# Optimization experiments

Hardware: AMD Instinct MI355X
Metric: run time of the kernel (lower is better)

Reference implementation:

```python
import jax, jax.numpy as jnp
import numpy as np

N, E, IN, H, B, OUT = 50000, 800000, 256, 64, 4096, 2
EPS, NEG = 0.3, 0.3  # eps residual coeff, LeakyReLU negative slope


def _xav(key, shape, gain=1.414):
    std = gain * np.sqrt(2.0 / (shape[0] + shape[1]))
    return jax.random.normal(key, shape, jnp.float32) * np.float32(std)


def setup_inputs():
    key = jax.random.key(0)
    ks = jax.random.split(key, 32)
    inp = {}
    inp["h"] = jax.random.normal(ks[0], (N, IN), jnp.float32)
    for i, name in enumerate(["src1", "dst1", "src2", "dst2", "src3", "dst3"]):
        inp[name] = jax.random.randint(ks[1 + i], (E,), 0, N, jnp.int32)
    inp["nodes"] = jax.random.randint(ks[7], (B,), 0, N, jnp.int32)
    inp["t1_w"] = _xav(ks[8], (H, IN))
    inp["t1_b"] = jnp.zeros((H,), jnp.float32)
    for i in range(3):
        inp[f"gw1_{i+1}"] = _xav(ks[9 + i], (1, 2 * H))
        inp[f"gb1_{i+1}"] = jnp.zeros((1,), jnp.float32)
        inp[f"hw1_{i+1}"] = _xav(ks[12 + i], (H, H))
        inp[f"gw2_{i+1}"] = _xav(ks[15 + i], (1, 6 * H))
        inp[f"gb2_{i+1}"] = jnp.zeros((1,), jnp.float32)
        inp[f"hw2_{i+1}"] = _xav(ks[18 + i], (3 * H, H))
    inp["t2_w"] = _xav(ks[21], (64, 7 * H + IN))
    inp["t2_b"] = jnp.zeros((64,), jnp.float32)
    inp["t3_w"] = _xav(ks[22], (OUT, 64))
    inp["t3_b"] = jnp.zeros((OUT,), jnp.float32)
    return inp


def _leaky(x):
    return jnp.where(x >= 0, x, NEG * x)


def _deg_norm(dst):
    # symmetric degree normalization d_i = 1/sqrt(deg_i) (FAGCN-style ndata['d'])
    deg = jax.ops.segment_sum(jnp.ones(dst.shape, jnp.float32), dst, num_segments=N)
    return jnp.where(deg > 0, jax.lax.rsqrt(jnp.maximum(deg, 1.0)), 0.0)


def _layer(h, src, dst, gw, gb, d):
    # a = tanh(gate(cat[h_dst, h_src])): split gate weight to avoid [E,2D] concat
    D = h.shape[1]
    a = jnp.tanh(h[dst] @ gw[0, :D] + h[src] @ gw[0, D:] + gb[0])  # [E]
    e = a * d[dst] * d[src]                                        # [E]
    # z_i = sum_{(src->i)} h_src * e  (DGL u_mul_e + sum)
    return jax.ops.segment_sum(h[src] * e[:, None], dst, num_segments=N)


def reference(h, t1_w, t1_b,
              gw1_1, gb1_1, hw1_1, gw1_2, gb1_2, hw1_2, gw1_3, gb1_3, hw1_3,
              gw2_1, gb2_1, hw2_1, gw2_2, gb2_2, hw2_2, gw2_3, gb2_3, hw2_3,
              t2_w, t2_b, t3_w, t3_b,
              src1, dst1, src2, dst2, src3, dst3, nodes):
    d1, d2, d3 = _deg_norm(dst1), _deg_norm(dst2), _deg_norm(dst3)
    raw0 = h
    x = _leaky(h @ t1_w.T + t1_b)                   # [N, H]
    raw1 = x
    h1_1 = _leaky((EPS * raw1 + _layer(x, src1, dst1, gw1_1, gb1_1, d1)) @ hw1_1)
    h1_2 = _leaky((EPS * raw1 + _layer(x, src2, dst2, gw1_2, gb1_2, d2)) @ hw1_2)
    h1_3 = _leaky((EPS * raw1 + _layer(x, src3, dst3, gw1_3, gb1_3, d3)) @ hw1_3)
    raw2 = jnp.concatenate([h1_1, h1_2, h1_3], axis=1)  # [N, 3H]
    h2_1 = _leaky((EPS * raw2 + _layer(raw2, src1, dst1, gw2_1, gb2_1, d1)) @ hw2_1)
    h2_2 = _leaky((EPS * raw2 + _layer(raw2, src2, dst2, gw2_2, gb2_2, d2)) @ hw2_2)
    h2_3 = _leaky((EPS * raw2 + _layer(raw2, src3, dst3, gw2_3, gb2_3, d3)) @ hw2_3)
    final = jnp.concatenate([h2_1, h2_2, h2_3, raw0, raw1, raw2], axis=1)  # [N, 7H+IN]
    nf = final[nodes]                                # [B, 7H+IN]
    s64 = _leaky(nf @ t2_w.T + t2_b)                 # [B, 64]
    scores = s64 @ t3_w.T + t3_b                     # [B, OUT]
    return scores, s64
```

## Files before the change

kernel.cpp:

```cpp
#include <hip/hip_runtime.h>

#define NN 50000
#define EE 800000
#define BB 4096
#define NB 512
#define BW 98
#define CAP 2176
#define CH 128

#define OFF_T1W 0
#define OFF_T1B 16384
#define OFF_GW1 16448
#define OFF_GB1 16832
#define OFF_HW1 16848
#define OFF_GW2 29136
#define OFF_GB2 30288
#define OFF_HW2 30304
#define OFF_T2W 67168
#define OFF_T2B 112224
#define OFF_T3W 112288
#define OFF_T3B 112416
#define WTOT    112418

#define WB_T1W  0
#define WB_HW1T 16384
#define WB_HW2T 28672
#define WB_T2W  65536
#define WB_TOT  110592

typedef __attribute__((ext_vector_type(8))) short bf16x8;
typedef __attribute__((ext_vector_type(4))) float f32x4;

__device__ __forceinline__ float bf2f(unsigned short u) {
    return __uint_as_float(((unsigned int)u) << 16);
}
__device__ __forceinline__ unsigned short f2bf(float f) {
    unsigned int u = __float_as_uint(f);
    u = (u + 0x7fffu + ((u >> 16) & 1u)) >> 16;
    return (unsigned short)u;
}
__device__ __forceinline__ float leakyf(float v) { return v >= 0.f ? v : 0.3f * v; }
__device__ __forceinline__ float tanh_fast(float v) {
    float e = __expf(2.f * v);
    return 1.f - 2.f / (e + 1.f);
}
__device__ __forceinline__ int rfl(int v) { return __builtin_amdgcn_readfirstlane(v); }

__global__ void k_sniff(const unsigned short* __restrict__ hs, int* __restrict__ flag) {
    int lane = threadIdx.x;
    unsigned short s = hs[2 * lane];
    int ef = (s >> 7) & 0xFF;
    unsigned long long m = __ballot(ef >= 100 && ef <= 132);
    if (lane == 0) flag[0] = (__popcll(m) >= 40) ? 0 : 1;
}

__global__ __launch_bounds__(1024) void k_convert(
    const int* __restrict__ fl,
    const void* t1w, const void* t1b,
    const void* gw1a, const void* gw1b, const void* gw1c,
    const void* gb1a, const void* gb1b, const void* gb1c,
    const void* hw1a, const void* hw1b, const void* hw1c,
    const void* gw2a, const void* gw2b, const void* gw2c,
    const void* gb2a, const void* gb2b, const void* gb2c,
    const void* hw2a, const void* hw2b, const void* hw2c,
    const void* t2w, const void* t2b, const void* t3w, const void* t3b,
    float* __restrict__ fw) {
    const int starts[24] = {0, 16384, 16448, 16576, 16704, 16832, 16833, 16834,
                            16848, 20944, 25040, 29136, 29520, 29904, 30288, 30289, 30290,
                            30304, 42592, 54880, 67168, 112224, 112288, 112416};
    const int cnts[24] = {16384, 64, 128, 128, 128, 1, 1, 1, 4096, 4096, 4096,
                          384, 384, 384, 1, 1, 1, 12288, 12288, 12288, 45056, 64, 128, 2};
    const void* sp[24] = {t1w, t1b, gw1a, gw1b, gw1c, gb1a, gb1b, gb1c, hw1a, hw1b, hw1c,
                          gw2a, gw2b, gw2c, gb2a, gb2b, gb2c, hw2a, hw2b, hw2c, t2w, t2b, t3w, t3b};
    int isf32 = fl[0];
    int idx = blockIdx.x * 1024 + threadIdx.x;
    if (idx >= WTOT) return;
    float v = 0.f;
#pragma unroll
    for (int k = 0; k < 24; ++k) {
        int lo = idx - starts[k];
        if (lo >= 0 && lo < cnts[k])
            v = isf32 ? ((const float*)sp[k])[lo] : bf2f(((const unsigned short*)sp[k])[lo]);
    }
    fw[idx] = v;
}

__global__ __launch_bounds__(256) void k_convert16(const int* __restrict__ fl, const void* t1w,
                                                   const void* hw1a, const void* hw1b, const void* hw1c,
                                                   const void* hw2a, const void* hw2b, const void* hw2c,
                                                   const void* t2w, unsigned short* __restrict__ wb) {
    int idx = blockIdx.x * 256 + threadIdx.x;
    if (idx >= WB_TOT) return;
    int isf32 = fl[0];
    const void* p;
    int srci;
    if (idx < WB_HW1T) {
        p = t1w; srci = idx;
    } else if (idx < WB_HW2T) {
        int rel = idx - WB_HW1T;
        int set = rel >> 12, r2 = rel & 4095;
        int jj = r2 >> 6, kk = r2 & 63;
        p = set == 0 ? hw1a : (set == 1 ? hw1b : hw1c);
        srci = kk * 64 + jj;
    } else if (idx < WB_T2W) {
        int rel = idx - WB_HW2T;
        int set = rel / 12288, r2 = rel % 12288;
        int n = r2 / 192, k = r2 % 192;
        p = set == 0 ? hw2a : (set == 1 ? hw2b : hw2c);
        srci = k * 64 + n;
    } else {
        p = t2w; srci = idx - WB_T2W;
    }
    wb[idx] = isf32 ? f2bf(((const float*)p)[srci]) : ((const unsigned short*)p)[srci];
}

__global__ __launch_bounds__(256) void k_bucketA(const int* __restrict__ s0, const int* __restrict__ s1,
                                                 const int* __restrict__ s2, const int* __restrict__ d0,
                                                 const int* __restrict__ d1, const int* __restrict__ d2,
                                                 int* __restrict__ gcur, unsigned int* __restrict__ tmp) {
    int set = blockIdx.y;
    const int* ss = set == 0 ? s0 : (set == 1 ? s1 : s2);
    const int* dd = set == 0 ? d0 : (set == 1 ? d1 : d2);
    __shared__ int hist[NB];
    __shared__ int lcur[NB];
    int tid = threadIdx.x;
    for (int i = tid; i < NB; i += 256) { hist[i] = 0; lcur[i] = 0; }
    __syncthreads();
    int e0 = blockIdx.x * (EE / CH);
    int e1 = e0 + (EE / CH);
    for (int t = e0 + tid; t < e1; t += 256)
        atomicAdd(&hist[dd[t] / BW], 1);
    __syncthreads();
    for (int b = tid; b < NB; b += 256) {
        int hh = hist[b];
        if (hh > 0) hist[b] = atomicAdd(&gcur[set * NB + b], hh);
    }
    __syncthreads();
    unsigned int* tp = tmp + (size_t)set * NB * CAP;
    for (int t = e0 + tid; t < e1; t += 256) {
        int d = dd[t], s = ss[t];
        int b = d / BW;
        int r = atomicAdd(&lcur[b], 1);
        int pos = hist[b] + r;
        if (pos < CAP) tp[(size_t)b * CAP + pos] = (unsigned)s | ((unsigned)(d - b * BW) << 16);
    }
}

__global__ __launch_bounds__(256) void k_rowptr(const int* __restrict__ gcur,
                                                const unsigned int* __restrict__ tmp,
                                                int* __restrict__ deg, int* __restrict__ rowptr,
                                                float* __restrict__ g1, float* __restrict__ g2) {
    int b = blockIdx.x, set = blockIdx.y;
    int nb = b * BW;
    if (nb >= NN) return;
    __shared__ int hist[BW];
    __shared__ int rp[BW];
    int tid = threadIdx.x;
    int nv = NN - nb < BW ? NN - nb : BW;
    if (tid < BW) hist[tid] = 0;
    __syncthreads();
    int cnt = gcur[set * NB + b];
    if (cnt > CAP) cnt = CAP;
    const unsigned int* tp = tmp + (size_t)set * NB * CAP + (size_t)b * CAP;
    for (int j = tid; j < cnt; j += 256) atomicAdd(&hist[tp[j] >> 16], 1);
    __syncthreads();
    if (tid == 0) {
        int run = 0;
        for (int i = 0; i < nv; ++i) { rp[i] = run; run += hist[i]; }
    }
    __syncthreads();
    if (tid < nv) {
        int dg = hist[tid];
        size_t n = (size_t)set * NN + nb + tid;
        deg[n] = dg;
        rowptr[n] = b * CAP + rp[tid];
        float v = dg > 0 ? rsqrtf((float)dg) : 0.f;
        g1[n * 4 + 2] = v;
        g2[n * 4 + 2] = v;
    }
}

__global__ __launch_bounds__(256) void k_input(const int* __restrict__ fl,
                                               const void* __restrict__ hB,
                                               const unsigned short* __restrict__ wb,
                                               const float* __restrict__ fw,
                                               unsigned short* __restrict__ x16,
                                               float4* __restrict__ g1v4) {
    __shared__ float xt[16][65];
    int tid = threadIdx.x, lane = tid & 63, wid = tid >> 6;
    int m = lane & 15, q = lane >> 4;
    int node0 = blockIdx.x * 16;
    int isf32 = fl[0];
    f32x4 acc = {0.f, 0.f, 0.f, 0.f};
    const unsigned short* bsrc = wb + WB_T1W + ((size_t)(wid * 16 + m)) * 256 + q * 8;
    if (isf32) {
        const float* ap = (const float*)hB + (size_t)(node0 + m) * 256 + q * 8;
        for (int k0 = 0; k0 < 256; k0 += 32) {
            float4 f0 = *(const float4*)(ap + k0);
            float4 f1 = *(const float4*)(ap + k0 + 4);
            bf16x8 a;
            a[0] = (short)f2bf(f0.x); a[1] = (short)f2bf(f0.y);
            a[2] = (short)f2bf(f0.z); a[3] = (short)f2bf(f0.w);
            a[4] = (short)f2bf(f1.x); a[5] = (short)f2bf(f1.y);
            a[6] = (short)f2bf(f1.z); a[7] = (short)f2bf(f1.w);
            bf16x8 b = *(const bf16x8*)(bsrc + k0);
            acc = __builtin_amdgcn_mfma_f32_16x16x32_bf16(a, b, acc, 0, 0, 0);
        }
    } else {
        const unsigned short* ap = (const unsigned short*)hB + (size_t)(node0 + m) * 256 + q * 8;
        for (int k0 = 0; k0 < 256; k0 += 32) {
            bf16x8 a = *(const bf16x8*)(ap + k0);
            bf16x8 b = *(const bf16x8*)(bsrc + k0);
            acc = __builtin_amdgcn_mfma_f32_16x16x32_bf16(a, b, acc, 0, 0, 0);
        }
    }
    int gcol = wid * 16 + m;
    float bias = fw[OFF_T1B + gcol];
#pragma unroll
    for (int r = 0; r < 4; ++r) {
        int row = q * 4 + r;
        float v = leakyf(acc[r] + bias);
        x16[(size_t)(node0 + row) * 64 + gcol] = f2bf(v);
        xt[row][gcol] = v;
    }
    __syncthreads();
    int nl = wid * 4 + q;
    int node = node0 + nl;
    float xv[4];
#pragma unroll
    for (int r = 0; r < 4; ++r) xv[r] = xt[nl][m + 16 * r];
#pragma unroll
    for (int set = 0; set < 3; ++set) {
        const float* gw = fw + OFF_GW1 + set * 128;
        float pd = 0.f, ps = 0.f;
#pragma unroll
        for (int r = 0; r < 4; ++r) {
            int c = m + 16 * r;
            pd = fmaf(xv[r], gw[c], pd);
            ps = fmaf(xv[r], gw[64 + c], ps);
        }
        pd += __shfl_xor(pd, 1); ps += __shfl_xor(ps, 1);
        pd += __shfl_xor(pd, 2); ps += __shfl_xor(ps, 2);
        pd += __shfl_xor(pd, 4); ps += __shfl_xor(ps, 4);
        pd += __shfl_xor(pd, 8); ps += __shfl_xor(ps, 8);
        if (m == 0) {
            float2* p = (float2*)&g1v4[(size_t)set * NN + node];
            *p = make_float2(ps, pd);
        }
    }
}

__global__ __launch_bounds__(256) void k_bucketB(const int* __restrict__ gcur,
                                                 const unsigned int* __restrict__ tmp,
                                                 const int* __restrict__ rowptr,
                                                 const float4* __restrict__ g1v4,
                                                 const float* __restrict__ fw,
                                                 unsigned int* __restrict__ csr) {
    int b = blockIdx.x, set = blockIdx.y;
    int nb = b * BW;
    if (nb >= NN) return;
    __shared__ float4 gdw[BW];
    __shared__ int cur[BW];
    __shared__ int rpl[BW];
    int tid = threadIdx.x;
    int nv = NN - nb < BW ? NN - nb : BW;
    if (tid < nv) {
        gdw[tid] = g1v4[(size_t)set * NN + nb + tid];
        rpl[tid] = rowptr[(size_t)set * NN + nb + tid];
        cur[tid] = 0;
    }
    __syncthreads();
    int cnt = gcur[set * NB + b];
    if (cnt > CAP) cnt = CAP;
    float gbv = fw[OFF_GB1 + set];
    const float4* gv = g1v4 + (size_t)set * NN;
    const unsigned int* tp = tmp + (size_t)set * NB * CAP + (size_t)b * CAP;
    unsigned int* cp = csr + (size_t)set * NB * CAP;
    for (int j = tid; j < cnt; j += 256) {
        unsigned rec = tp[j];
        int s = rec & 0xFFFF;
        int dl = rec >> 16;
        float4 gs = gv[s];
        float4 gd = gdw[dl];
        float a = tanh_fast(gd.y + gs.x + gbv);
        float e = a * gd.z * gs.z;
        int rank = atomicAdd(&cur[dl], 1);
        cp[rpl[dl] + rank] = (unsigned)s | ((unsigned)f2bf(e) << 16);
    }
}

__global__ __launch_bounds__(1024) void k_layer1(const unsigned short* __restrict__ x16,
                                                 const unsigned int* __restrict__ csr,
                                                 const int* __restrict__ rowptr,
                                                 const int* __restrict__ deg,
                                                 const float* __restrict__ fw,
                                                 const unsigned short* __restrict__ wb,
                                                 unsigned short* __restrict__ raw2_16,
                                                 float4* __restrict__ g2v4) {
    __shared__ unsigned short tb[3][16][72];
    __shared__ unsigned short r2l[16][200];
    int tid = threadIdx.x, lane = tid & 63, wid = tid >> 6;
    int half = lane >> 5, c = lane & 31;
    int node = blockIdx.x * 16 + wid;
    unsigned xres = *(const unsigned*)(x16 + (size_t)node * 64 + 2 * c);
    float xr0 = bf2f((unsigned short)(xres & 0xFFFF));
    float xr1 = bf2f((unsigned short)(xres >> 16));
#pragma unroll
    for (int set = 0; set < 3; ++set) {
        int start = rfl(rowptr[(size_t)set * NN + node]);
        int cnt = rfl(deg[(size_t)set * NN + node]);
        const unsigned int* cs = csr + (size_t)set * NB * CAP + start;
        float a0 = 0.f, a1 = 0.f;
        int j = 0;
        for (; j + 8 <= cnt; j += 8) {
#pragma unroll
            for (int k = 0; k < 4; ++k) {
                unsigned rec = cs[j + 2 * k + half];
                float e = bf2f((unsigned short)(rec >> 16));
                unsigned u = *(const unsigned*)(x16 + (size_t)(rec & 0xFFFF) * 64 + 2 * c);
                a0 = fmaf(bf2f((unsigned short)(u & 0xFFFF)), e, a0);
                a1 = fmaf(bf2f((unsigned short)(u >> 16)), e, a1);
            }
        }
        for (; j + 2 <= cnt; j += 2) {
            unsigned rec = cs[j + half];
            float e = bf2f((unsigned short)(rec >> 16));
            unsigned u = *(const unsigned*)(x16 + (size_t)(rec & 0xFFFF) * 64 + 2 * c);
            a0 = fmaf(bf2f((unsigned short)(u & 0xFFFF)), e, a0);
            a1 = fmaf(bf2f((unsigned short)(u >> 16)), e, a1);
        }
        if (j < cnt && half == 0) {
            unsigned rec = cs[j];
            float e = bf2f((unsigned short)(rec >> 16));
            unsigned u = *(const unsigned*)(x16 + (size_t)(rec & 0xFFFF) * 64 + 2 * c);
            a0 = fmaf(bf2f((unsigned short)(u & 0xFFFF)), e, a0);
            a1 = fmaf(bf2f((unsigned short)(u >> 16)), e, a1);
        }
        a0 += __shfl_xor(a0, 32);
        a1 += __shfl_xor(a1, 32);
        if (half == 0) {
            unsigned p = ((unsigned)f2bf(fmaf(0.3f, xr1, a1)) << 16) |
                         (unsigned)f2bf(fmaf(0.3f, xr0, a0));
            *(unsigned*)&tb[set][wid][2 * c] = p;
        }
    }
    __syncthreads();
    int m = lane & 15, q = lane >> 4;
    if (wid < 12) {
        int set = wid >> 2, sw = wid & 3;
        f32x4 c4 = {0.f, 0.f, 0.f, 0.f};
        const unsigned short* bp = wb + WB_HW1T + set * 4096 + (sw * 16 + m) * 64 + q * 8;
#pragma unroll
        for (int k0 = 0; k0 < 64; k0 += 32) {
            bf16x8 a = *(const bf16x8*)&tb[set][m][k0 + q * 8];
            bf16x8 b = *(const bf16x8*)(bp + k0);
            c4 = __builtin_amdgcn_mfma_f32_16x16x32_bf16(a, b, c4, 0, 0, 0);
        }
        int gcol = sw * 16 + m;
#pragma unroll
        for (int r = 0; r < 4; ++r) {
            int row = q * 4 + r;
            unsigned short v = f2bf(leakyf(c4[r]));
            raw2_16[(size_t)(blockIdx.x * 16 + row) * 192 + set * 64 + gcol] = v;
            r2l[row][set * 64 + gcol] = v;
        }
    }
    __syncthreads();
    float pd[3] = {0.f, 0.f, 0.f}, ps[3] = {0.f, 0.f, 0.f};
    float rv[3];
#pragma unroll
    for (int t = 0; t < 3; ++t) rv[t] = bf2f(r2l[wid][lane * 3 + t]);
#pragma unroll
    for (int set = 0; set < 3; ++set) {
        const float* g = fw + OFF_GW2 + set * 384;
#pragma unroll
        for (int t = 0; t < 3; ++t) {
            int cc = lane * 3 + t;
            pd[set] = fmaf(rv[t], g[cc], pd[set]);
            ps[set] = fmaf(rv[t], g[192 + cc], ps[set]);
        }
    }
#pragma unroll
    for (int mm = 32; mm >= 1; mm >>= 1) {
#pragma unroll
        for (int set = 0; set < 3; ++set) {
            pd[set] += __shfl_xor(pd[set], mm);
            ps[set] += __shfl_xor(ps[set], mm);
        }
    }
    if (lane == 0) {
#pragma unroll
        for (int set = 0; set < 3; ++set) {
            float2* p = (float2*)&g2v4[(size_t)set * NN + node];
            *p = make_float2(ps[set], pd[set]);
        }
    }
}

__global__ __launch_bounds__(256) void k_mark(const int* __restrict__ nodes, int* __restrict__ mark,
                                              int* __restrict__ slotof, int* __restrict__ slotnode,
                                              int* __restrict__ cnt) {
    int b = blockIdx.x * 256 + threadIdx.x;
    if (b < BB) {
        int n = nodes[b];
        if (atomicCAS(&mark[n], 0, 1) == 0) {
            int s = atomicAdd(cnt, 1);
            slotof[n] = s;
            slotnode[s] = n;
        }
    }
}

__global__ __launch_bounds__(1024) void k_layer2(const unsigned short* __restrict__ raw2_16,
                                                 const unsigned int* __restrict__ csr,
                                                 const int* __restrict__ rowptr,
                                                 const int* __restrict__ deg,
                                                 const float4* __restrict__ g2v4,
                                                 const float* __restrict__ fw,
                                                 const int* __restrict__ slotnode,
                                                 const int* __restrict__ cntp,
                                                 float* __restrict__ z2) {
    int set = blockIdx.y;
    int tid = threadIdx.x, lane = tid & 63, wid = tid >> 6;
    int half = lane >> 5, c = lane & 31;
    int slot = blockIdx.x * 16 + wid;
    if (slot >= cntp[0]) return;
    int node = rfl(slotnode[slot]);
    int start = rfl(rowptr[(size_t)set * NN + node]);
    int cnt = rfl(deg[(size_t)set * NN + node]);
    float4 gn = g2v4[(size_t)set * NN + node];
    float pdv = gn.y, dnd = gn.z;
    float gbv = fw[OFF_GB2 + set];
    const unsigned int* cs = csr + (size_t)set * NB * CAP + start;
    const float4* gv = g2v4 + (size_t)set * NN;
    float a[6] = {0.f, 0.f, 0.f, 0.f, 0.f, 0.f};
    int j = 0;
    for (; j + 2 <= cnt; j += 2) {
        unsigned rec = cs[j + half];
        int s = rec & 0xFFFF;
        float4 g = gv[s];
        float e = tanh_fast(pdv + g.x + gbv) * dnd * g.z;
        const unsigned short* r = raw2_16 + (size_t)s * 192;
#pragma unroll
        for (int blk = 0; blk < 3; ++blk) {
            unsigned u = *(const unsigned*)(r + blk * 64 + 2 * c);
            a[2 * blk] = fmaf(bf2f((unsigned short)(u & 0xFFFF)), e, a[2 * blk]);
            a[2 * blk + 1] = fmaf(bf2f((unsigned short)(u >> 16)), e, a[2 * blk + 1]);
        }
    }
    if (j < cnt && half == 0) {
        unsigned rec = cs[j];
        int s = rec & 0xFFFF;
        float4 g = gv[s];
        float e = tanh_fast(pdv + g.x + gbv) * dnd * g.z;
        const unsigned short* r = raw2_16 + (size_t)s * 192;
#pragma unroll
        for (int blk = 0; blk < 3; ++blk) {
            unsigned u = *(const unsigned*)(r + blk * 64 + 2 * c);
            a[2 * blk] = fmaf(bf2f((unsigned short)(u & 0xFFFF)), e, a[2 * blk]);
            a[2 * blk + 1] = fmaf(bf2f((unsigned short)(u >> 16)), e, a[2 * blk + 1]);
        }
    }
#pragma unroll
    for (int i = 0; i < 6; ++i) a[i] += __shfl_xor(a[i], 32);
    if (half == 0) {
        float* z = z2 + (size_t)slot * 576 + (size_t)set * 192;
#pragma unroll
        for (int blk = 0; blk < 3; ++blk) {
            z[blk * 64 + 2 * c] = a[2 * blk];
            z[blk * 64 + 2 * c + 1] = a[2 * blk + 1];
        }
    }
}

__global__ __launch_bounds__(256) void k_final(const int* __restrict__ fl,
                                               const int* __restrict__ nodes,
                                               const int* __restrict__ slotof,
                                               const float* __restrict__ z2,
                                               const unsigned short* __restrict__ raw2_16,
                                               const unsigned short* __restrict__ x16,
                                               const void* __restrict__ hB,
                                               const float* __restrict__ fw,
                                               const unsigned short* __restrict__ wb,
                                               void* __restrict__ outv) {
    __shared__ unsigned short nfb[16][712];
    __shared__ unsigned short tbb[16][200];
    __shared__ float sarr[16][64];
    __shared__ int nd[16], sl[16];
    int tid = threadIdx.x, lane = tid & 63, wid = tid >> 6;
    int m = lane & 15, q = lane >> 4;
    int b0 = blockIdx.x * 16;
    int isf32 = fl[0];
    if (tid < 16) {
        int n = nodes[b0 + tid];
        nd[tid] = n;
        sl[tid] = slotof[n];
    }
    __syncthreads();
    for (int idx = tid; idx < 16 * 256; idx += 256) {
        int row = idx >> 8, c = idx & 255;
        size_t hi = (size_t)nd[row] * 256 + c;
        nfb[row][192 + c] = isf32 ? f2bf(((const float*)hB)[hi]) : ((const unsigned short*)hB)[hi];
    }
    for (int idx = tid; idx < 16 * 64; idx += 256) {
        int row = idx >> 6, c = idx & 63;
        nfb[row][448 + c] = x16[(size_t)nd[row] * 64 + c];
    }
    for (int idx = tid; idx < 16 * 192; idx += 256) {
        int row = idx / 192, c = idx % 192;
        nfb[row][512 + c] = raw2_16[(size_t)nd[row] * 192 + c];
    }
    for (int set = 0; set < 3; ++set) {
        __syncthreads();
        for (int idx = tid; idx < 16 * 192; idx += 256) {
            int row = idx / 192, c = idx % 192;
            float r2 = bf2f(nfb[row][512 + c]);
            tbb[row][c] = f2bf(fmaf(0.3f, r2, z2[(size_t)sl[row] * 576 + set * 192 + c]));
        }
        __syncthreads();
        f32x4 c4 = {0.f, 0.f, 0.f, 0.f};
        const unsigned short* bp = wb + WB_HW2T + set * 12288 + (wid * 16 + m) * 192 + q * 8;
#pragma unroll
        for (int k0 = 0; k0 < 192; k0 += 32) {
            bf16x8 a = *(const bf16x8*)&tbb[m][k0 + q * 8];
            bf16x8 bf = *(const bf16x8*)(bp + k0);
            c4 = __builtin_amdgcn_mfma_f32_16x16x32_bf16(a, bf, c4, 0, 0, 0);
        }
        int col = wid * 16 + m;
#pragma unroll
        for (int r = 0; r < 4; ++r)
            nfb[q * 4 + r][set * 64 + col] = f2bf(leakyf(c4[r]));
    }
    __syncthreads();
    f32x4 c4 = {0.f, 0.f, 0.f, 0.f};
    const unsigned short* bp = wb + WB_T2W + (wid * 16 + m) * 704 + q * 8;
#pragma unroll
    for (int k0 = 0; k0 < 704; k0 += 32) {
        bf16x8 a = *(const bf16x8*)&nfb[m][k0 + q * 8];
        bf16x8 bf = *(const bf16x8*)(bp + k0);
        c4 = __builtin_amdgcn_mfma_f32_16x16x32_bf16(a, bf, c4, 0, 0, 0);
    }
    int col = wid * 16 + m;
    float bias = fw[OFF_T2B + col];
#pragma unroll
    for (int r = 0; r < 4; ++r) {
        int row = q * 4 + r;
        float sv = leakyf(c4[r] + bias);
        sarr[row][col] = sv;
        size_t oi = 8192 + (size_t)(b0 + row) * 64 + col;
        if (isf32) ((float*)outv)[oi] = sv;
        else ((unsigned short*)outv)[oi] = f2bf(sv);
    }
    __syncthreads();
    if (tid < 32) {
        int row = tid >> 1, oc = tid & 1;
        float acc2 = fw[OFF_T3B + oc];
        const float* tw = fw + OFF_T3W + oc * 64;
#pragma unroll 8
        for (int c = 0; c < 64; ++c) acc2 = fmaf(sarr[row][c], tw[c], acc2);
        size_t oi = (size_t)(b0 + row) * 2 + oc;
        if (isf32) ((float*)outv)[oi] = acc2;
        else ((unsigned short*)outv)[oi] = f2bf(acc2);
    }
}

extern "C" void kernel_launch(void* const* d_in, const int* in_sizes, int n_in,
                              void* d_out, int out_size, void* d_ws, size_t ws_size,
                              hipStream_t stream) {
    const void* h = d_in[0];
    const int* src1 = (const int*)d_in[1];
    const int* dst1 = (const int*)d_in[2];
    const int* src2 = (const int*)d_in[3];
    const int* dst2 = (const int*)d_in[4];
    const int* src3 = (const int*)d_in[5];
    const int* dst3 = (const int*)d_in[6];
    const int* nodes = (const int*)d_in[7];

    char* w = (char*)d_ws;
    size_t off = 0;
    auto carve = [&](size_t bytes) -> void* {
        void* p = w + off;
        off += (bytes + 255) & ~(size_t)255;
        return p;
    };
    int* flag = (int*)carve(256);
    int* gcur = (int*)carve((size_t)3 * NB * 4);
    int* mark = (int*)carve((size_t)NN * 4);
    int* cntp = (int*)carve(256);
    int* deg = (int*)carve((size_t)3 * NN * 4);
    int* rowptr = (int*)carve((size_t)3 * NN * 4);
    float4* g1v4 = (float4*)carve((size_t)3 * NN * 16);
    float4* g2v4 = (float4*)carve((size_t)3 * NN * 16);
    unsigned int* tmp = (unsigned int*)carve((size_t)3 * NB * CAP * 4);
    unsigned int* csr = (unsigned int*)carve((size_t)3 * NB * CAP * 4);
    float* fw = (float*)carve((size_t)WTOT * 4);
    unsigned short* wb = (unsigned short*)carve((size_t)WB_TOT * 2);
    unsigned short* x16 = (unsigned short*)carve((size_t)NN * 64 * 2);
    unsigned short* raw2_16 = (unsigned short*)carve((size_t)NN * 192 * 2);
    int* slotof = (int*)carve((size_t)NN * 4);
    int* slotnode = (int*)carve((size_t)BB * 4);
    float* z2 = (float*)carve((size_t)BB * 576 * 4);

    size_t zbytes = (size_t)((char*)cntp - (char*)gcur) + 256;
    hipMemsetAsync(gcur, 0, zbytes, stream);

    k_sniff<<<1, 64, 0, stream>>>((const unsigned short*)h, flag);
    k_convert<<<(WTOT + 1023) / 1024, 1024, 0, stream>>>(
        flag, d_in[8], d_in[9],
        d_in[10], d_in[16], d_in[22],
        d_in[11], d_in[17], d_in[23],
        d_in[12], d_in[18], d_in[24],
        d_in[13], d_in[19], d_in[25],
        d_in[14], d_in[20], d_in[26],
        d_in[15], d_in[21], d_in[27],
        d_in[28], d_in[29], d_in[30], d_in[31], fw);
    k_convert16<<<(WB_TOT + 255) / 256, 256, 0, stream>>>(flag, d_in[8],
                                                          d_in[12], d_in[18], d_in[24],
                                                          d_in[15], d_in[21], d_in[27],
                                                          d_in[28], wb);

    dim3 gch(CH, 3);
    k_bucketA<<<gch, 256, 0, stream>>>(src1, src2, src3, dst1, dst2, dst3, gcur, tmp);
    dim3 gb(NB, 3);
    k_rowptr<<<gb, 256, 0, stream>>>(gcur, tmp, deg, rowptr, (float*)g1v4, (float*)g2v4);

    k_input<<<3125, 256, 0, stream>>>(flag, h, wb, fw, x16, g1v4);
    k_bucketB<<<gb, 256, 0, stream>>>(gcur, tmp, rowptr, g1v4, fw, csr);
    k_mark<<<(BB + 255) / 256, 256, 0, stream>>>(nodes, mark, slotof, slotnode, cntp);

    k_layer1<<<3125, 1024, 0, stream>>>(x16, csr, rowptr, deg, fw, wb, raw2_16, g2v4);
    dim3 gl2(BB / 16, 3);
    k_layer2<<<gl2, 1024, 0, stream>>>(raw2_16, csr, rowptr, deg, g2v4, fw, slotnode, cntp, z2);
    k_final<<<BB / 16, 256, 0, stream>>>(flag, nodes, slotof, z2, raw2_16, x16, h, fw, wb, d_out);
}
```

Before: 413.6 us.

## Fuse layer-2 aggregation into final kernel, merge convert kernels, inline dtype sniff

Folds the dtype sniff into each kernel that needs it, merges the two weight-conversion kernels into one launch, and drops the dedup/mark pass. Layer-2 aggregation now runs directly inside the final kernel per batch node, with no z2 round-trip. Layer-1 aggregation is regathered with 8-byte loads and 4 edges per wave step. This cuts launches, the memset and z2 traffic, at the cost of recomputing aggregation for duplicate batch nodes and running fewer blocks in the final kernel.

```diff
diff --git a/kernel.cpp b/kernel.cpp
--- a/kernel.cpp
+++ b/kernel.cpp
@@ -21,6 +21,7 @@
 #define OFF_T3W 112288
 #define OFF_T3B 112416
 #define WTOT    112418
+#define WPAD    112640
 
 #define WB_T1W  0
 #define WB_HW1T 16384
@@ -46,16 +47,16 @@
 }
 __device__ __forceinline__ int rfl(int v) { return __builtin_amdgcn_readfirstlane(v); }
 
-__global__ void k_sniff(const unsigned short* __restrict__ hs, int* __restrict__ flag) {
-    int lane = threadIdx.x;
+__device__ __forceinline__ int sniff_wave(const unsigned short* hs) {
+    int lane = threadIdx.x & 63;
     unsigned short s = hs[2 * lane];
     int ef = (s >> 7) & 0xFF;
     unsigned long long m = __ballot(ef >= 100 && ef <= 132);
-    if (lane == 0) flag[0] = (__popcll(m) >= 40) ? 0 : 1;
-}
-
-__global__ __launch_bounds__(1024) void k_convert(
-    const int* __restrict__ fl,
+    return (__popcll(m) >= 40) ? 0 : 1;
+}
+
+__global__ __launch_bounds__(256) void k_convert(
+    const unsigned short* __restrict__ hs,
     const void* t1w, const void* t1b,
     const void* gw1a, const void* gw1b, const void* gw1c,
     const void* gb1a, const void* gb1b, const void* gb1c,
@@ -64,7 +65,7 @@
     const void* gb2a, const void* gb2b, const void* gb2c,
     const void* hw2a, const void* hw2b, const void* hw2c,
     const void* t2w, const void* t2b, const void* t3w, const void* t3b,
-    float* __restrict__ fw) {
+    float* __restrict__ fw, unsigned short* __restrict__ wb) {
     const int starts[24] = {0, 16384, 16448, 16576, 16704, 16832, 16833, 16834,
                             16848, 20944, 25040, 29136, 29520, 29904, 30288, 30289, 30290,
                             30304, 42592, 54880, 67168, 112224, 112288, 112416};
@@ -72,46 +73,40 @@
                           384, 384, 384, 1, 1, 1, 12288, 12288, 12288, 45056, 64, 128, 2};
     const void* sp[24] = {t1w, t1b, gw1a, gw1b, gw1c, gb1a, gb1b, gb1c, hw1a, hw1b, hw1c,
                           gw2a, gw2b, gw2c, gb2a, gb2b, gb2c, hw2a, hw2b, hw2c, t2w, t2b, t3w, t3b};
-    int isf32 = fl[0];
-    int idx = blockIdx.x * 1024 + threadIdx.x;
-    if (idx >= WTOT) return;
-    float v = 0.f;
-#pragma unroll
-    for (int k = 0; k < 24; ++k) {
-        int lo = idx - starts[k];
-        if (lo >= 0 && lo < cnts[k])
-            v = isf32 ? ((const float*)sp[k])[lo] : bf2f(((const unsigned short*)sp[k])[lo]);
-    }
-    fw[idx] = v;
-}
-
-__global__ __launch_bounds__(256) void k_convert16(const int* __restrict__ fl, const void* t1w,
-                                                   const void* hw1a, const void* hw1b, const void* hw1c,
-                                                   const void* hw2a, const void* hw2b, const void* hw2c,
-                                                   const void* t2w, unsigned short* __restrict__ wb) {
+    int isf32 = sniff_wave(hs);
     int idx = blockIdx.x * 256 + threadIdx.x;
-    if (idx >= WB_TOT) return;
-    int isf32 = fl[0];
-    const void* p;
-    int srci;
-    if (idx < WB_HW1T) {
-        p = t1w; srci = idx;
-    } else if (idx < WB_HW2T) {
-        int rel = idx - WB_HW1T;
-        int set = rel >> 12, r2 = rel & 4095;
-        int jj = r2 >> 6, kk = r2 & 63;
-        p = set == 0 ? hw1a : (set == 1 ? hw1b : hw1c);
-        srci = kk * 64 + jj;
-    } else if (idx < WB_T2W) {
-        int rel = idx - WB_HW2T;
-        int set = rel / 12288, r2 = rel % 12288;
-        int n = r2 / 192, k = r2 % 192;
-        p = set == 0 ? hw2a : (set == 1 ? hw2b : hw2c);
-        srci = k * 64 + n;
-    } else {
-        p = t2w; srci = idx - WB_T2W;
-    }
-    wb[idx] = isf32 ? f2bf(((const float*)p)[srci]) : ((const unsigned short*)p)[srci];
+    if (idx < WTOT) {
+        float v = 0.f;
+#pragma unroll
+        for (int k = 0; k < 24; ++k) {
+            int lo = idx - starts[k];
+            if (lo >= 0 && lo < cnts[k])
+                v = isf32 ? ((const float*)sp[k])[lo] : bf2f(((const unsigned short*)sp[k])[lo]);
+        }
+        fw[idx] = v;
+    } else if (idx >= WPAD && idx < WPAD + WB_TOT) {
+        int i2 = idx - WPAD;
+        const void* p;
+        int srci;
+        if (i2 < WB_HW1T) {
+            p = t1w; srci = i2;
+        } else if (i2 < WB_HW2T) {
+            int rel = i2 - WB_HW1T;
+            int set = rel >> 12, r2 = rel & 4095;
+            int jj = r2 >> 6, kk = r2 & 63;
+            p = set == 0 ? hw1a : (set == 1 ? hw1b : hw1c);
+            srci = kk * 64 + jj;
+        } else if (i2 < WB_T2W) {
+            int rel = i2 - WB_HW2T;
+            int set = rel / 12288, r2 = rel % 12288;
+            int n = r2 / 192, k = r2 % 192;
+            p = set == 0 ? hw2a : (set == 1 ? hw2b : hw2c);
+            srci = k * 64 + n;
+        } else {
+            p = t2w; srci = i2 - WB_T2W;
+        }
+        wb[i2] = isf32 ? f2bf(((const float*)p)[srci]) : ((const unsigned short*)p)[srci];
+    }
 }
 
 __global__ __launch_bounds__(256) void k_bucketA(const int* __restrict__ s0, const int* __restrict__ s1,
@@ -180,8 +175,7 @@
     }
 }
 
-__global__ __launch_bounds__(256) void k_input(const int* __restrict__ fl,
-                                               const void* __restrict__ hB,
+__global__ __launch_bounds__(256) void k_input(const void* __restrict__ hB,
                                                const unsigned short* __restrict__ wb,
                                                const float* __restrict__ fw,
                                                unsigned short* __restrict__ x16,
@@ -190,7 +184,7 @@
     int tid = threadIdx.x, lane = tid & 63, wid = tid >> 6;
     int m = lane & 15, q = lane >> 4;
     int node0 = blockIdx.x * 16;
-    int isf32 = fl[0];
+    int isf32 = sniff_wave((const unsigned short*)hB);
     f32x4 acc = {0.f, 0.f, 0.f, 0.f};
     const unsigned short* bsrc = wb + WB_T1W + ((size_t)(wid * 16 + m)) * 256 + q * 8;
     if (isf32) {
@@ -300,48 +294,54 @@
     __shared__ unsigned short tb[3][16][72];
     __shared__ unsigned short r2l[16][200];
     int tid = threadIdx.x, lane = tid & 63, wid = tid >> 6;
-    int half = lane >> 5, c = lane & 31;
+    int g = lane >> 4, f = lane & 15;
     int node = blockIdx.x * 16 + wid;
-    unsigned xres = *(const unsigned*)(x16 + (size_t)node * 64 + 2 * c);
-    float xr0 = bf2f((unsigned short)(xres & 0xFFFF));
-    float xr1 = bf2f((unsigned short)(xres >> 16));
 #pragma unroll
     for (int set = 0; set < 3; ++set) {
         int start = rfl(rowptr[(size_t)set * NN + node]);
         int cnt = rfl(deg[(size_t)set * NN + node]);
         const unsigned int* cs = csr + (size_t)set * NB * CAP + start;
-        float a0 = 0.f, a1 = 0.f;
+        float a0 = 0.f, a1 = 0.f, a2 = 0.f, a3 = 0.f;
         int j = 0;
         for (; j + 8 <= cnt; j += 8) {
 #pragma unroll
-            for (int k = 0; k < 4; ++k) {
-                unsigned rec = cs[j + 2 * k + half];
+            for (int k2 = 0; k2 < 2; ++k2) {
+                unsigned rec = cs[j + 4 * k2 + g];
                 float e = bf2f((unsigned short)(rec >> 16));
-                unsigned u = *(const unsigned*)(x16 + (size_t)(rec & 0xFFFF) * 64 + 2 * c);
-                a0 = fmaf(bf2f((unsigned short)(u & 0xFFFF)), e, a0);
-                a1 = fmaf(bf2f((unsigned short)(u >> 16)), e, a1);
+                uint2 u = *(const uint2*)(x16 + (size_t)(rec & 0xFFFF) * 64 + 4 * f);
+                a0 = fmaf(bf2f((unsigned short)(u.x & 0xFFFF)), e, a0);
+                a1 = fmaf(bf2f((unsigned short)(u.x >> 16)), e, a1);
+                a2 = fmaf(bf2f((unsigned short)(u.y & 0xFFFF)), e, a2);
+                a3 = fmaf(bf2f((unsigned short)(u.y >> 16)), e, a3);
             }
         }
-        for (; j + 2 <= cnt; j += 2) {
-            unsigned rec = cs[j + half];
-            float e = bf2f((unsigned short)(rec >> 16));
-            unsigned u = *(const unsigned*)(x16 + (size_t)(rec & 0xFFFF) * 64 + 2 * c);
-            a0 = fmaf(bf2f((unsigned short)(u & 0xFFFF)), e, a0);
-            a1 = fmaf(bf2f((unsigned short)(u >> 16)), e, a1);
-        }
-        if (j < cnt && half == 0) {
-            unsigned rec = cs[j];
-            float e = bf2f((unsigned short)(rec >> 16));
-            unsigned u = *(const unsigned*)(x16 + (size_t)(rec & 0xFFFF) * 64 + 2 * c);
-            a0 = fmaf(bf2f((unsigned short)(u & 0xFFFF)), e, a0);
-            a1 = fmaf(bf2f((unsigned short)(u >> 16)), e, a1);
-        }
-        a0 += __shfl_xor(a0, 32);
-        a1 += __shfl_xor(a1, 32);
-        if (half == 0) {
-            unsigned p = ((unsigned)f2bf(fmaf(0.3f, xr1, a1)) << 16) |
-                         (unsigned)f2bf(fmaf(0.3f, xr0, a0));
-            *(unsigned*)&tb[set][wid][2 * c] = p;
+#pragma unroll
+        for (int t = 0; t < 2; ++t) {
+            int idx = j + 4 * t + g;
+            if (idx < cnt) {
+                unsigned rec = cs[idx];
+                float e = bf2f((unsigned short)(rec >> 16));
+                uint2 u = *(const uint2*)(x16 + (size_t)(rec & 0xFFFF) * 64 + 4 * f);
+                a0 = fmaf(bf2f((unsigned short)(u.x & 0xFFFF)), e, a0);
+                a1 = fmaf(bf2f((unsigned short)(u.x >> 16)), e, a1);
+                a2 = fmaf(bf2f((unsigned short)(u.y & 0xFFFF)), e, a2);
+                a3 = fmaf(bf2f((unsigned short)(u.y >> 16)), e, a3);
+            }
+        }
+        a0 += __shfl_xor(a0, 16); a0 += __shfl_xor(a0, 32);
+        a1 += __shfl_xor(a1, 16); a1 += __shfl_xor(a1, 32);
+        a2 += __shfl_xor(a2, 16); a2 += __shfl_xor(a2, 32);
+        a3 += __shfl_xor(a3, 16); a3 += __shfl_xor(a3, 32);
+        if (g == 0) {
+            uint2 ur = *(const uint2*)(x16 + (size_t)node * 64 + 4 * f);
+            float t0 = fmaf(0.3f, bf2f((unsigned short)(ur.x & 0xFFFF)), a0);
+            float t1 = fmaf(0.3f, bf2f((unsigned short)(ur.x >> 16)), a1);
+            float t2 = fmaf(0.3f, bf2f((unsigned short)(ur.y & 0xFFFF)), a2);
+            float t3 = fmaf(0.3f, bf2f((unsigned short)(ur.y >> 16)), a3);
+            uint2 pk;
+            pk.x = (unsigned)f2bf(t0) | ((unsigned)f2bf(t1) << 16);
+            pk.y = (unsigned)f2bf(t2) | ((unsigned)f2bf(t3) << 16);
+            *(uint2*)&tb[set][wid][4 * f] = pk;
         }
     }
     __syncthreads();
@@ -372,12 +372,12 @@
     for (int t = 0; t < 3; ++t) rv[t] = bf2f(r2l[wid][lane * 3 + t]);
 #pragma unroll
     for (int set = 0; set < 3; ++set) {
-        const float* g = fw + OFF_GW2 + set * 384;
+        const float* gg = fw + OFF_GW2 + set * 384;
 #pragma unroll
         for (int t = 0; t < 3; ++t) {
             int cc = lane * 3 + t;
-            pd[set] = fmaf(rv[t], g[cc], pd[set]);
-            ps[set] = fmaf(rv[t], g[192 + cc], ps[set]);
+            pd[set] = fmaf(rv[t], gg[cc], pd[set]);
+            ps[set] = fmaf(rv[t], gg[192 + cc], ps[set]);
         }
     }
 #pragma unroll
@@ -397,159 +397,132 @@
     }
 }
 
-__global__ __launch_bounds__(256) void k_mark(const int* __restrict__ nodes, int* __restrict__ mark,
-                                              int* __restrict__ slotof, int* __restrict__ slotnode,
-                                              int* __restrict__ cnt) {
-    int b = blockIdx.x * 256 + threadIdx.x;
-    if (b < BB) {
-        int n = nodes[b];
-        if (atomicCAS(&mark[n], 0, 1) == 0) {
-            int s = atomicAdd(cnt, 1);
-            slotof[n] = s;
-            slotnode[s] = n;
-        }
-    }
-}
-
-__global__ __launch_bounds__(1024) void k_layer2(const unsigned short* __restrict__ raw2_16,
-                                                 const unsigned int* __restrict__ csr,
-                                                 const int* __restrict__ rowptr,
-                                                 const int* __restrict__ deg,
-                                                 const float4* __restrict__ g2v4,
-                                                 const float* __restrict__ fw,
-                                                 const int* __restrict__ slotnode,
-                                                 const int* __restrict__ cntp,
-                                                 float* __restrict__ z2) {
-    int set = blockIdx.y;
+__global__ __launch_bounds__(1024) void k_final(const int* __restrict__ nodes,
+                                                const unsigned short* __restrict__ raw2_16,
+                                                const unsigned short* __restrict__ x16,
+                                                const void* __restrict__ hB,
+                                                const unsigned int* __restrict__ csr,
+                                                const int* __restrict__ rowptr,
+                                                const int* __restrict__ deg,
+                                                const float4* __restrict__ g2v4,
+                                                const float* __restrict__ fw,
+                                                const unsigned short* __restrict__ wb,
+                                                void* __restrict__ outv) {
+    __shared__ unsigned short nfb[16][712];
+    __shared__ unsigned short tbb3[16][584];
+    __shared__ float sarr[16][64];
+    __shared__ int nd[16];
     int tid = threadIdx.x, lane = tid & 63, wid = tid >> 6;
-    int half = lane >> 5, c = lane & 31;
-    int slot = blockIdx.x * 16 + wid;
-    if (slot >= cntp[0]) return;
-    int node = rfl(slotnode[slot]);
-    int start = rfl(rowptr[(size_t)set * NN + node]);
-    int cnt = rfl(deg[(size_t)set * NN + node]);
-    float4 gn = g2v4[(size_t)set * NN + node];
-    float pdv = gn.y, dnd = gn.z;
-    float gbv = fw[OFF_GB2 + set];
-    const unsigned int* cs = csr + (size_t)set * NB * CAP + start;
-    const float4* gv = g2v4 + (size_t)set * NN;
-    float a[6] = {0.f, 0.f, 0.f, 0.f, 0.f, 0.f};
-    int j = 0;
-    for (; j + 2 <= cnt; j += 2) {
-        unsigned rec = cs[j + half];
-        int s = rec & 0xFFFF;
-        float4 g = gv[s];
-        float e = tanh_fast(pdv + g.x + gbv) * dnd * g.z;
-        const unsigned short* r = raw2_16 + (size_t)s * 192;
-#pragma unroll
-        for (int blk = 0; blk < 3; ++blk) {
-            unsigned u = *(const unsigned*)(r + blk * 64 + 2 * c);
-            a[2 * blk] = fmaf(bf2f((unsigned short)(u & 0xFFFF)), e, a[2 * blk]);
-            a[2 * blk + 1] = fmaf(bf2f((unsigned short)(u >> 16)), e, a[2 * blk + 1]);
-        }
-    }
-    if (j < cnt && half == 0) {
-        unsigned rec = cs[j];
-        int s = rec & 0xFFFF;
-        float4 g = gv[s];
-        float e = tanh_fast(pdv + g.x + gbv) * dnd * g.z;
-        const unsigned short* r = raw2_16 + (size_t)s * 192;
-#pragma unroll
-        for (int blk = 0; blk < 3; ++blk) {
-            unsigned u = *(const unsigned*)(r + blk * 64 + 2 * c);
-            a[2 * blk] = fmaf(bf2f((unsigned short)(u & 0xFFFF)), e, a[2 * blk]);
-            a[2 * blk + 1] = fmaf(bf2f((unsigned short)(u >> 16)), e, a[2 * blk + 1]);
-        }
-    }
-#pragma unroll
-    for (int i = 0; i < 6; ++i) a[i] += __shfl_xor(a[i], 32);
-    if (half == 0) {
-        float* z = z2 + (size_t)slot * 576 + (size_t)set * 192;
-#pragma unroll
-        for (int blk = 0; blk < 3; ++blk) {
-            z[blk * 64 + 2 * c] = a[2 * blk];
-            z[blk * 64 + 2 * c + 1] = a[2 * blk + 1];
-        }
-    }
-}
-
-__global__ __launch_bounds__(256) void k_final(const int* __restrict__ fl,
-                                               const int* __restrict__ nodes,
-                                               const int* __restrict__ slotof,
-                                               const float* __restrict__ z2,
-                                               const unsigned short* __restrict__ raw2_16,
-                                               const unsigned short* __restrict__ x16,
-                                               const void* __restrict__ hB,
-                                               const float* __restrict__ fw,
-                                               const unsigned short* __restrict__ wb,
-                                               void* __restrict__ outv) {
-    __shared__ unsigned short nfb[16][712];
-    __shared__ unsigned short tbb[16][200];
-    __shared__ float sarr[16][64];
-    __shared__ int nd[16], sl[16];
-    int tid = threadIdx.x, lane = tid & 63, wid = tid >> 6;
-    int m = lane & 15, q = lane >> 4;
     int b0 = blockIdx.x * 16;
-    int isf32 = fl[0];
-    if (tid < 16) {
-        int n = nodes[b0 + tid];
-        nd[tid] = n;
-        sl[tid] = slotof[n];
-    }
-    __syncthreads();
-    for (int idx = tid; idx < 16 * 256; idx += 256) {
+    int isf32 = sniff_wave((const unsigned short*)hB);
+    if (tid < 16) nd[tid] = nodes[b0 + tid];
+    __syncthreads();
+    for (int idx = tid; idx < 16 * 256; idx += 1024) {
         int row = idx >> 8, c = idx & 255;
         size_t hi = (size_t)nd[row] * 256 + c;
         nfb[row][192 + c] = isf32 ? f2bf(((const float*)hB)[hi]) : ((const unsigned short*)hB)[hi];
     }
-    for (int idx = tid; idx < 16 * 64; idx += 256) {
+    for (int idx = tid; idx < 16 * 64; idx += 1024) {
         int row = idx >> 6, c = idx & 63;
         nfb[row][448 + c] = x16[(size_t)nd[row] * 64 + c];
     }
-    for (int idx = tid; idx < 16 * 192; idx += 256) {
+    for (int idx = tid; idx < 16 * 192; idx += 1024) {
         int row = idx / 192, c = idx % 192;
         nfb[row][512 + c] = raw2_16[(size_t)nd[row] * 192 + c];
     }
-    for (int set = 0; set < 3; ++set) {
-        __syncthreads();
-        for (int idx = tid; idx < 16 * 192; idx += 256) {
-            int row = idx / 192, c = idx % 192;
-            float r2 = bf2f(nfb[row][512 + c]);
-            tbb[row][c] = f2bf(fmaf(0.3f, r2, z2[(size_t)sl[row] * 576 + set * 192 + c]));
-        }
-        __syncthreads();
+    __syncthreads();
+    {
+        int node = rfl(nd[wid]);
+        int half = lane >> 5, c = lane & 31;
+#pragma unroll
+        for (int set = 0; set < 3; ++set) {
+            int start = rfl(rowptr[(size_t)set * NN + node]);
+            int cnt = rfl(deg[(size_t)set * NN + node]);
+            float4 gn = g2v4[(size_t)set * NN + node];
+            float pdv = gn.y, dnd = gn.z;
+            float gbv = fw[OFF_GB2 + set];
+            const unsigned int* cs = csr + (size_t)set * NB * CAP + start;
+            const float4* gv = g2v4 + (size_t)set * NN;
+            float a[6] = {0.f, 0.f, 0.f, 0.f, 0.f, 0.f};
+            int j = 0;
+            for (; j + 2 <= cnt; j += 2) {
+                unsigned rec = cs[j + half];
+                int s = rec & 0xFFFF;
+                float4 gg = gv[s];
+                float e = tanh_fast(pdv + gg.x + gbv) * dnd * gg.z;
+                const unsigned short* r = raw2_16 + (size_t)s * 192;
+#pragma unroll
+                for (int blk = 0; blk < 3; ++blk) {
+                    unsigned u = *(const unsigned*)(r + blk * 64 + 2 * c);
+                    a[2 * blk] = fmaf(bf2f((unsigned short)(u & 0xFFFF)), e, a[2 * blk]);
+                    a[2 * blk + 1] = fmaf(bf2f((unsigned short)(u >> 16)), e, a[2 * blk + 1]);
+                }
+            }
+            if (j < cnt && half == 0) {
+                unsigned rec = cs[j];
+                int s = rec & 0xFFFF;
+                float4 gg = gv[s];
+                float e = tanh_fast(pdv + gg.x + gbv) * dnd * gg.z;
+                const unsigned short* r = raw2_16 + (size_t)s * 192;
+#pragma unroll
+                for (int blk = 0; blk < 3; ++blk) {
+                    unsigned u = *(const unsigned*)(r + blk * 64 + 2 * c);
+                    a[2 * blk] = fmaf(bf2f((unsigned short)(u & 0xFFFF)), e, a[2 * blk]);
+                    a[2 * blk + 1] = fmaf(bf2f((unsigned short)(u >> 16)), e, a[2 * blk + 1]);
+                }
+            }
+#pragma unroll
+            for (int i = 0; i < 6; ++i) a[i] += __shfl_xor(a[i], 32);
+            if (half == 0) {
+#pragma unroll
+                for (int blk = 0; blk < 3; ++blk) {
+                    int fc0 = blk * 64 + 2 * c;
+                    float r20 = bf2f(nfb[wid][512 + fc0]);
+                    float r21 = bf2f(nfb[wid][512 + fc0 + 1]);
+                    tbb3[wid][set * 192 + fc0] = f2bf(fmaf(0.3f, r20, a[2 * blk]));
+                    tbb3[wid][set * 192 + fc0 + 1] = f2bf(fmaf(0.3f, r21, a[2 * blk + 1]));
+                }
+            }
+        }
+    }
+    __syncthreads();
+    int m = lane & 15, q = lane >> 4;
+    if (wid < 12) {
+        int set = wid >> 2, sw = wid & 3;
         f32x4 c4 = {0.f, 0.f, 0.f, 0.f};
-        const unsigned short* bp = wb + WB_HW2T + set * 12288 + (wid * 16 + m) * 192 + q * 8;
+        const unsigned short* bp = wb + WB_HW2T + set * 12288 + (sw * 16 + m) * 192 + q * 8;
 #pragma unroll
         for (int k0 = 0; k0 < 192; k0 += 32) {
-            bf16x8 a = *(const bf16x8*)&tbb[m][k0 + q * 8];
+            bf16x8 a = *(const bf16x8*)&tbb3[m][set * 192 + k0 + q * 8];
             bf16x8 bf = *(const bf16x8*)(bp + k0);
             c4 = __builtin_amdgcn_mfma_f32_16x16x32_bf16(a, bf, c4, 0, 0, 0);
         }
-        int col = wid * 16 + m;
+        int col = sw * 16 + m;
 #pragma unroll
         for (int r = 0; r < 4; ++r)
             nfb[q * 4 + r][set * 64 + col] = f2bf(leakyf(c4[r]));
     }
     __syncthreads();
-    f32x4 c4 = {0.f, 0.f, 0.f, 0.f};
-    const unsigned short* bp = wb + WB_T2W + (wid * 16 + m) * 704 + q * 8;
-#pragma unroll
-    for (int k0 = 0; k0 < 704; k0 += 32) {
-        bf16x8 a = *(const bf16x8*)&nfb[m][k0 + q * 8];
-        bf16x8 bf = *(const bf16x8*)(bp + k0);
-        c4 = __builtin_amdgcn_mfma_f32_16x16x32_bf16(a, bf, c4, 0, 0, 0);
-    }
-    int col = wid * 16 + m;
-    float bias = fw[OFF_T2B + col];
-#pragma unroll
-    for (int r = 0; r < 4; ++r) {
-        int row = q * 4 + r;
-        float sv = leakyf(c4[r] + bias);
-        sarr[row][col] = sv;
-        size_t oi = 8192 + (size_t)(b0 + row) * 64 + col;
-        if (isf32) ((float*)outv)[oi] = sv;
-        else ((unsigned short*)outv)[oi] = f2bf(sv);
+    if (wid < 4) {
+        f32x4 c4 = {0.f, 0.f, 0.f, 0.f};
+        const unsigned short* bp = wb + WB_T2W + (wid * 16 + m) * 704 + q * 8;
+#pragma unroll
+        for (int k0 = 0; k0 < 704; k0 += 32) {
+            bf16x8 a = *(const bf16x8*)&nfb[m][k0 + q * 8];
+            bf16x8 bf = *(const bf16x8*)(bp + k0);
+            c4 = __builtin_amdgcn_mfma_f32_16x16x32_bf16(a, bf, c4, 0, 0, 0);
+        }
+        int col = wid * 16 + m;
+        float bias = fw[OFF_T2B + col];
+#pragma unroll
+        for (int r = 0; r < 4; ++r) {
+            int row = q * 4 + r;
+            float sv = leakyf(c4[r] + bias);
+            sarr[row][col] = sv;
+            size_t oi = 8192 + (size_t)(b0 + row) * 64 + col;
+            if (isf32) ((float*)outv)[oi] = sv;
+            else ((unsigned short*)outv)[oi] = f2bf(sv);
+        }
     }
     __syncthreads();
     if (tid < 32) {
@@ -583,10 +556,7 @@
         off += (bytes + 255) & ~(size_t)255;
         return p;
     };
-    int* flag = (int*)carve(256);
     int* gcur = (int*)carve((size_t)3 * NB * 4);
-    int* mark = (int*)carve((size_t)NN * 4);
-    int* cntp = (int*)carve(256);
     int* deg = (int*)carve((size_t)3 * NN * 4);
     int* rowptr = (int*)carve((size_t)3 * NN * 4);
     float4* g1v4 = (float4*)carve((size_t)3 * NN * 16);
@@ -597,39 +567,29 @@
     unsigned short* wb = (unsigned short*)carve((size_t)WB_TOT * 2);
     unsigned short* x16 = (unsigned short*)carve((size_t)NN * 64 * 2);
     unsigned short* raw2_16 = (unsigned short*)carve((size_t)NN * 192 * 2);
-    int* slotof = (int*)carve((size_t)NN * 4);
-    int* slotnode = (int*)carve((size_t)BB * 4);
-    float* z2 = (float*)carve((size_t)BB * 576 * 4);
-
-    size_t zbytes = (size_t)((char*)cntp - (char*)gcur) + 256;
-    hipMemsetAsync(gcur, 0, zbytes, stream);
-
-    k_sniff<<<1, 64, 0, stream>>>((const unsigned short*)h, flag);
-    k_convert<<<(WTOT + 1023) / 1024, 1024, 0, stream>>>(
-        flag, d_in[8], d_in[9],
+
+    hipMemsetAsync(gcur, 0, (size_t)3 * NB * 4, stream);
+
+    k_convert<<<(WPAD + WB_TOT) / 256, 256, 0, stream>>>(
+        (const unsigned short*)h,
+        d_in[8], d_in[9],
         d_in[10], d_in[16], d_in[22],
         d_in[11], d_in[17], d_in[23],
         d_in[12], d_in[18], d_in[24],
         d_in[13], d_in[19], d_in[25],
         d_in[14], d_in[20], d_in[26],
         d_in[15], d_in[21], d_in[27],
-        d_in[28], d_in[29], d_in[30], d_in[31], fw);
-    k_convert16<<<(WB_TOT + 255) / 256, 256, 0, stream>>>(flag, d_in[8],
-                                                          d_in[12], d_in[18], d_in[24],
-                                                          d_in[15], d_in[21], d_in[27],
-                                                          d_in[28], wb);
+        d_in[28], d_in[29], d_in[30], d_in[31], fw, wb);
 
     dim3 gch(CH, 3);
     k_bucketA<<<gch, 256, 0, stream>>>(src1, src2, src3, dst1, dst2, dst3, gcur, tmp);
     dim3 gb(NB, 3);
     k_rowptr<<<gb, 256, 0, stream>>>(gcur, tmp, deg, rowptr, (float*)g1v4, (float*)g2v4);
 
-    k_input<<<3125, 256, 0, stream>>>(flag, h, wb, fw, x16, g1v4);
+    k_input<<<3125, 256, 0, stream>>>(h, wb, fw, x16, g1v4);
     k_bucketB<<<gb, 256, 0, stream>>>(gcur, tmp, rowptr, g1v4, fw, csr);
-    k_mark<<<(BB + 255) / 256, 256, 0, stream>>>(nodes, mark, slotof, slotnode, cntp);
 
     k_layer1<<<3125, 1024, 0, stream>>>(x16, csr, rowptr, deg, fw, wb, raw2_16, g2v4);
-    dim3 gl2(BB / 16, 3);
-    k_layer2<<<gl2, 1024, 0, stream>>>(raw2_16, csr, rowptr, deg, g2v4, fw, slotnode, cntp, z2);
-    k_final<<<BB / 16, 256, 0, stream>>>(flag, nodes, slotof, z2, raw2_16, x16, h, fw, wb, d_out);
-}
+    k_final<<<BB / 16, 1024, 0, stream>>>(nodes, raw2_16, x16, h, csr, rowptr, deg, g2v4,
+                                          fw, wb, d_out);
+}
```

After: 377.8 us. 8.7% less time.
